# Performance work log

Hardware: AMD Instinct MI355X
Metric: run time of the kernel (lower is better)

The kernel has to match this reference:

```python
import jax, jax.numpy as jnp
import numpy as np

D_POINTS = 256
D_MODEL = 512
B, N = 8, 2048


def setup_inputs() -> dict:
    key = jax.random.key(0)
    ks = jax.random.split(key, 6)
    s_in = 1.0 / np.sqrt(D_POINTS)
    s_mid = 1.0 / np.sqrt(D_MODEL)
    return {
        "features": jax.random.normal(ks[0], (B, N, D_POINTS), dtype=jnp.float32),
        "Wq": jax.random.uniform(ks[1], (D_POINTS, D_MODEL), jnp.float32, -s_in, s_in),
        "Wk": jax.random.uniform(ks[2], (D_POINTS, D_MODEL), jnp.float32, -s_in, s_in),
        "Wv": jax.random.uniform(ks[3], (D_POINTS, D_MODEL), jnp.float32, -s_in, s_in),
        "W2": jax.random.uniform(ks[4], (D_MODEL, D_POINTS), jnp.float32, -s_mid, s_mid),
        "b2": jax.random.uniform(ks[5], (D_POINTS,), jnp.float32, -s_mid, s_mid),
    }


def reference(features, Wq, Wk, Wv, W2, b2):
    # features: [B, N, d_points]
    q = jnp.einsum("bnd,dm->bnm", features, Wq)  # [B, N, d_model]
    k = jnp.einsum("bnd,dm->bnm", features, Wk)
    v = jnp.einsum("bnd,dm->bnm", features, Wv)
    scale = 1.0 / np.sqrt(k.shape[-1]).astype(np.float32)
    attn = jax.nn.softmax(jnp.einsum("bnm,bkm->bnk", q, k) * scale, axis=-1)  # [B, N, N]
    res = jnp.einsum("bnk,bkm->bnm", attn, v)  # [B, N, d_model]
    res = jnp.einsum("bnm,md->bnd", res, W2) + b2  # fc2 -> [B, N, d_points]
    res = jax.nn.leaky_relu(res, negative_slope=0.2)
    return res + features
```

## Files before the change

kernel.cpp:

```cpp
#include <hip/hip_runtime.h>
#include <cstdint>

#define NBATCH 8
#define NSEQ   2048
#define NROWS  16384

typedef __attribute__((ext_vector_type(4))) float  f32x4;
typedef __attribute__((ext_vector_type(8))) short  short8;
typedef __attribute__((ext_vector_type(8))) __bf16 bf16x8;
typedef __attribute__((ext_vector_type(8))) _Float16 h8;

#define XB_OFF   0ul
#define WALL_OFF 8388608ul
#define Q_OFF    9175040ul
#define K_OFF    25952256ul
#define VT_OFF   42729472ul
#define W2T_OFF  59506688ul
#define S_OFF    59768832ul

#define SCALE_Q 0.063758746f

__device__ __forceinline__ unsigned short f2bf(float f) {
  unsigned u = __builtin_bit_cast(unsigned, f);
  return (unsigned short)((u + 0x7fffu + ((u >> 16) & 1u)) >> 16);
}

__device__ __forceinline__ f32x4 mfma16(short8 a, short8 b, f32x4 c) {
  return __builtin_amdgcn_mfma_f32_16x16x32_bf16(
      __builtin_bit_cast(bf16x8, a), __builtin_bit_cast(bf16x8, b), c, 0, 0, 0);
}

__device__ __forceinline__ void glds16(const void* g, void* l) {
  __builtin_amdgcn_global_load_lds(
      (const __attribute__((address_space(1))) void*)g,
      (__attribute__((address_space(3))) void*)l, 16, 0, 0);
}

#define BAR_SYNC()                     \
  {                                    \
    __builtin_amdgcn_sched_barrier(0); \
    __builtin_amdgcn_s_barrier();      \
    __builtin_amdgcn_sched_barrier(0); \
  }
#define BAR_LGKM()                                           \
  {                                                          \
    asm volatile("s_waitcnt lgkmcnt(0)" ::: "memory");       \
    __builtin_amdgcn_sched_barrier(0);                       \
    __builtin_amdgcn_s_barrier();                            \
    __builtin_amdgcn_sched_barrier(0);                       \
  }
#define WAITV(N)                                                  \
  {                                                               \
    asm volatile("s_waitcnt vmcnt(" #N ")" ::: "memory");         \
    __builtin_amdgcn_sched_barrier(0);                            \
  }

__global__ __launch_bounds__(256, 4) void prep_kernel(
    const float* __restrict__ feat, const float* __restrict__ Wq,
    const float* __restrict__ Wk, const float* __restrict__ Wv,
    const float* __restrict__ W2, char* __restrict__ ws) {
  int tid = blockIdx.x * 256 + threadIdx.x;
  if (tid < 524288) {
    int r = tid >> 5, co = (tid & 31) * 8;
    const float* src = feat + (size_t)r * 256 + co;
    short8 v;
#pragma unroll
    for (int i = 0; i < 8; ++i) v[i] = (short)f2bf(src[i]);
    unsigned short* Xb = (unsigned short*)(ws + XB_OFF);
    *(short8*)(Xb + (size_t)r * 256 + (co ^ ((r & 7) << 3))) = v;
  } else if (tid < 917504) {
    int t2 = tid - 524288;
    int m = t2 >> 8, d = t2 & 255;
    int wsel = m >> 9, mm = m & 511;
    const float* W = (wsel == 0) ? Wq : ((wsel == 1) ? Wk : Wv);
    float v = W[(size_t)d * 512 + mm];
    if (wsel == 0) v *= SCALE_Q;
    unsigned short* Wall = (unsigned short*)(ws + WALL_OFF);
    Wall[(size_t)m * 256 + (d ^ ((m & 7) << 3))] = f2bf(v);
  } else {
    int t3 = tid - 917504;
    int d = t3 >> 9, c = t3 & 511;
    unsigned short* W2t = (unsigned short*)(ws + W2T_OFF);
    W2t[(size_t)d * 512 + c] = f2bf(W2[(size_t)c * 256 + d]);
  }
}

__global__ __launch_bounds__(256, 2) void proj_kernel(char* __restrict__ ws) {
  __shared__ char smem[65536];
  const int tid = threadIdx.x;
  const int l = tid & 63, w = tid >> 6;
  const int g = l >> 4, m16 = l & 15;
  const int orig = blockIdx.x;
  const int wgid = (orig & 7) * 192 + (orig >> 3);
  const int nt = wgid % 12, mtb = wgid / 12;
  const char* XbT = ws + XB_OFF + (size_t)mtb * 65536;
  const char* WallT = ws + WALL_OFF + (size_t)nt * 65536;

  auto stage = [&](int buf, int kt) {
#pragma unroll
    for (int j = 0; j < 4; ++j) {
      int idx = j * 256 + tid;
      int r = idx >> 3, p = idx & 7;
      glds16(XbT + r * 512 + kt * 128 + p * 16, smem + buf * 16384 + idx * 16);
      glds16(WallT + r * 512 + kt * 128 + p * 16,
             smem + 32768 + buf * 16384 + idx * 16);
    }
  };

  const int mr = (w >> 1) * 64, nr = (w & 1) * 64;
  const int fxor = (m16 & 7) << 4;
  const f32x4 fz = {0.f, 0.f, 0.f, 0.f};
  f32x4 acc[4][4];
#pragma unroll
  for (int i = 0; i < 4; ++i)
#pragma unroll
    for (int j = 0; j < 4; ++j) acc[i][j] = fz;

  stage(0, 0);
  int cur = 0;
#pragma unroll 1
  for (int kt = 0; kt < 4; ++kt) {
    if (kt < 3) {
      stage(cur ^ 1, kt + 1);
      WAITV(8);
    } else {
      WAITV(0);
    }
    BAR_SYNC();
    const char* Ab = smem + cur * 16384;
    const char* Bb = smem + 32768 + cur * 16384;
#pragma unroll
    for (int ks = 0; ks < 2; ++ks) {
      int off = (16 * g + 64 * ks) ^ fxor;
      short8 af[4], bf[4];
#pragma unroll
      for (int i = 0; i < 4; ++i)
        af[i] = *(const short8*)(Ab + (mr + i * 16 + m16) * 128 + off);
#pragma unroll
      for (int i = 0; i < 4; ++i)
        bf[i] = *(const short8*)(Bb + (nr + i * 16 + m16) * 128 + off);
#pragma unroll
      for (int mi = 0; mi < 4; ++mi)
#pragma unroll
        for (int ni = 0; ni < 4; ++ni)
          acc[mi][ni] = mfma16(af[mi], bf[ni], acc[mi][ni]);
    }
    BAR_LGKM();
    cur ^= 1;
  }

  const int colg = nt * 128 + nr;
  const int tcat = colg >> 9;
  const int cin_base = colg & 511;
  char* wbuf = smem + w * 2048;
  if (tcat < 2) {
    char* dst = ws + (tcat == 0 ? Q_OFF : K_OFF) +
                ((size_t)(mtb * 8 + (cin_base >> 6))) * 16384;
#pragma unroll
    for (int mi = 0; mi < 4; ++mi) {
#pragma unroll
      for (int ni = 0; ni < 4; ++ni)
#pragma unroll
        for (int j = 0; j < 4; ++j) {
          int r = g * 4 + j, c = ni * 16 + m16;
          *(unsigned short*)(wbuf + r * 128 + ((2 * c) ^ ((r & 7) << 4))) =
              f2bf(acc[mi][ni][j]);
        }
      asm volatile("s_waitcnt lgkmcnt(0)" ::: "memory");
      __builtin_amdgcn_sched_barrier(0);
#pragma unroll
      for (int s = 0; s < 2; ++s) {
        int cid = l + 64 * s;
        int r2 = cid >> 3, gi = cid & 7;
        short8 v = *(const short8*)(wbuf + r2 * 128 + gi * 16);
        int rt = mr + mi * 16 + r2;
        *(short8*)(dst + (size_t)rt * 128 + gi * 16) = v;
      }
    }
  } else {
    short8 grans[8];
#pragma unroll
    for (int mi = 0; mi < 4; ++mi) {
#pragma unroll
      for (int ni = 0; ni < 4; ++ni)
#pragma unroll
        for (int j = 0; j < 4; ++j) {
          int r = g * 4 + j, c = ni * 16 + m16;
          *(unsigned short*)(wbuf + r * 128 + ((2 * c) ^ ((r & 7) << 4))) =
              f2bf(acc[mi][ni][j]);
        }
      asm volatile("s_waitcnt lgkmcnt(0)" ::: "memory");
      __builtin_amdgcn_sched_barrier(0);
      unsigned short vals[16];
#pragma unroll
      for (int r2 = 0; r2 < 16; ++r2)
        vals[r2] = *(const unsigned short*)(wbuf + r2 * 128 +
                                            ((2 * l) ^ ((r2 & 7) << 4)));
      short8 v0, v1;
#pragma unroll
      for (int i2 = 0; i2 < 8; ++i2) {
        v0[i2] = (short)vals[i2];
        v1[i2] = (short)vals[8 + i2];
      }
      grans[2 * mi] = v0;
      grans[2 * mi + 1] = v1;
    }
    int cin = cin_base + l;
    int grow0 = mtb * 128 + mr;
    int bb = grow0 >> 11;
    int ktv = (grow0 & 2047) >> 6;
    char* vrow = ws + VT_OFF + (size_t)bb * 2097152 + (size_t)ktv * 65536 +
                 (size_t)cin * 128;
    const int fc = (cin & 7) << 4;
#pragma unroll
    for (int t = 0; t < 8; ++t)
      *(short8*)(vrow + ((t * 16) ^ fc)) = grans[t];
  }
}

__global__ __launch_bounds__(256, 2) void qk_kernel(
    const char* __restrict__ ws, char* __restrict__ Sb, int nb, int b0) {
  __shared__ char smem[65536];
  const int tid = threadIdx.x;
  const int bid = blockIdx.x;
  const int z = bid % nb, tile = bid / nb;
  const int mt = tile >> 4, ntq = tile & 15;
  const int b = b0 + z;
  const int l = tid & 63, w = tid >> 6;
  const int g = l >> 4, m16 = l & 15;
  const int fxor = (m16 & 7) << 4;
  const char* Qt = ws + Q_OFF + (size_t)(b * 16 + mt) * 131072;
  const char* Kt = ws + K_OFF + (size_t)(b * 16 + ntq) * 131072;

  auto stage = [&](int buf, int kt) {
#pragma unroll
    for (int j = 0; j < 4; ++j) {
      int idx = j * 256 + tid;
      glds16(Qt + (size_t)kt * 16384 + idx * 16, smem + buf * 16384 + idx * 16);
      glds16(Kt + (size_t)kt * 16384 + idx * 16,
             smem + 32768 + buf * 16384 + idx * 16);
    }
  };

  const int mr = (w >> 1) * 64, nr = (w & 1) * 64;
  const f32x4 fz = {0.f, 0.f, 0.f, 0.f};
  f32x4 acc[4][4];
#pragma unroll
  for (int i = 0; i < 4; ++i)
#pragma unroll
    for (int j = 0; j < 4; ++j) acc[i][j] = fz;

  stage(0, 0);
  int cur = 0;
#pragma unroll 1
  for (int kt = 0; kt < 8; ++kt) {
    if (kt < 7) {
      stage(cur ^ 1, kt + 1);
      WAITV(8);
    } else {
      WAITV(0);
    }
    BAR_SYNC();
    const char* Ab = smem + cur * 16384;
    const char* Bb = smem + 32768 + cur * 16384;
#pragma unroll
    for (int ks = 0; ks < 2; ++ks) {
      int off = (16 * g + 64 * ks) ^ fxor;
      short8 af[4], bf[4];
#pragma unroll
      for (int i = 0; i < 4; ++i)
        af[i] = *(const short8*)(Ab + (mr + i * 16 + m16) * 128 + off);
#pragma unroll
      for (int i = 0; i < 4; ++i)
        bf[i] = *(const short8*)(Bb + (nr + i * 16 + m16) * 128 + off);
#pragma unroll
      for (int mi = 0; mi < 4; ++mi)
#pragma unroll
        for (int ni = 0; ni < 4; ++ni)
          acc[mi][ni] = mfma16(af[mi], bf[ni], acc[mi][ni]);
    }
    BAR_LGKM();
    cur ^= 1;
  }

#pragma unroll
  for (int mi = 0; mi < 4; ++mi)
#pragma unroll
    for (int ni = 0; ni < 4; ++ni)
#pragma unroll
      for (int j = 0; j < 4; ++j) {
        int r = mr + mi * 16 + g * 4 + j, c = nr + ni * 16 + m16;
        *(unsigned short*)(smem + r * 272 + 2 * c) =
            __builtin_bit_cast(unsigned short, (_Float16)acc[mi][ni][j]);
      }
  BAR_LGKM();
  char* Sbt = Sb + (size_t)z * 8388608;
#pragma unroll
  for (int it = 0; it < 8; ++it) {
    int idx = it * 256 + tid;
    int r = idx >> 4, gi = idx & 15;
    int rg = mt * 2 + (r >> 6), ck = ntq * 2 + (gi >> 3);
    *(short8*)(Sbt + ((size_t)(rg * 32 + ck) * 64 + (r & 63)) * 128 +
               (gi & 7) * 16) = *(const short8*)(smem + r * 272 + gi * 16);
  }
}

__global__ __launch_bounds__(256, 8) void stats_kernel(char* __restrict__ Sb) {
  const int w = threadIdx.x >> 6, l = threadIdx.x & 63;
  const size_t row = (size_t)blockIdx.x * 4 + w;
  const int z = (int)(row >> 11), rloc = (int)(row & 2047);
  const int rg = rloc >> 6, r64 = rloc & 63;
  const int f = (rloc & 7) << 4;
  char* base = Sb + (size_t)z * 8388608 + (size_t)rg * 262144 +
               (size_t)r64 * 128;
  float sv[32];
#pragma unroll
  for (int i = 0; i < 4; ++i) {
    int idx = i * 64 + l;
    int ck = idx >> 3, gi = idx & 7;
    h8 hv = *(const h8*)(base + (size_t)ck * 8192 + gi * 16);
#pragma unroll
    for (int j = 0; j < 8; ++j) sv[i * 8 + j] = (float)hv[j];
  }
  float m = sv[0];
#pragma unroll
  for (int i = 1; i < 32; ++i) m = fmaxf(m, sv[i]);
  m = fmaxf(m, __shfl_xor(m, 1));
  m = fmaxf(m, __shfl_xor(m, 2));
  m = fmaxf(m, __shfl_xor(m, 4));
  m = fmaxf(m, __shfl_xor(m, 8));
  m = fmaxf(m, __shfl_xor(m, 16));
  m = fmaxf(m, __shfl_xor(m, 32));
  float sum = 0.f;
#pragma unroll
  for (int i = 0; i < 32; ++i) {
    float p = exp2f(sv[i] - m);
    sv[i] = p;
    sum += p;
  }
  sum += __shfl_xor(sum, 1);
  sum += __shfl_xor(sum, 2);
  sum += __shfl_xor(sum, 4);
  sum += __shfl_xor(sum, 8);
  sum += __shfl_xor(sum, 16);
  sum += __shfl_xor(sum, 32);
  const float rs = 1.0f / sum;
#pragma unroll
  for (int i = 0; i < 4; ++i) {
    int idx = i * 64 + l;
    int ck = idx >> 3, gi = idx & 7;
    short8 pk;
#pragma unroll
    for (int j = 0; j < 8; ++j) pk[j] = (short)f2bf(sv[i * 8 + j] * rs);
    *(short8*)(base + (size_t)ck * 8192 + ((gi * 16) ^ f)) = pk;
  }
}

__global__ __launch_bounds__(512, 2) void pv_kernel(
    const char* __restrict__ ws, const char* __restrict__ Sb,
    const float* __restrict__ feat, const float* __restrict__ b2,
    float* __restrict__ out, int nb, int b0) {
  __shared__ char smem[147456];
  const int tid = threadIdx.x;
  const int bid = blockIdx.x;
  const int z = bid % nb, mt64 = bid / nb;
  const int b = b0 + z;
  const int l = tid & 63, w = tid >> 6;
  const int g = l >> 4, m16 = l & 15;
  const int fxor = (m16 & 7) << 4;
  const char* Pr = Sb + (size_t)z * 8388608 + (size_t)mt64 * 262144;
  const char* Vt = ws + VT_OFF + (size_t)b * 2097152;

  auto stage = [&](int buf, int kt) {
    glds16(Pr + (size_t)kt * 8192 + tid * 16, smem + buf * 8192 + tid * 16);
#pragma unroll
    for (int j = 0; j < 8; ++j) {
      int idx = j * 512 + tid;
      glds16(Vt + (size_t)kt * 65536 + idx * 16,
             smem + 16384 + buf * 65536 + idx * 16);
    }
  };

  const f32x4 fz = {0.f, 0.f, 0.f, 0.f};
  f32x4 acc[4][4];
#pragma unroll
  for (int i = 0; i < 4; ++i)
#pragma unroll
    for (int j = 0; j < 4; ++j) acc[i][j] = fz;

  stage(0, 0);
  int cur = 0;
#pragma unroll 1
  for (int kt = 0; kt < 32; ++kt) {
    if (kt < 31) {
      stage(cur ^ 1, kt + 1);
      WAITV(9);
    } else {
      WAITV(0);
    }
    BAR_SYNC();
    const char* Ab = smem + cur * 8192;
    const char* Vb = smem + 16384 + cur * 65536 + w * 8192;
#pragma unroll
    for (int ks = 0; ks < 2; ++ks) {
      int off = (16 * g + 64 * ks) ^ fxor;
      short8 af[4], vf[4];
#pragma unroll
      for (int i = 0; i < 4; ++i)
        af[i] = *(const short8*)(Ab + (i * 16 + m16) * 128 + off);
#pragma unroll
      for (int i = 0; i < 4; ++i)
        vf[i] = *(const short8*)(Vb + (i * 16 + m16) * 128 + off);
#pragma unroll
      for (int mi = 0; mi < 4; ++mi)
#pragma unroll
        for (int ni = 0; ni < 4; ++ni)
          acc[mi][ni] = mfma16(af[mi], vf[ni], acc[mi][ni]);
    }
    BAR_LGKM();
    cur ^= 1;
  }

  char* Ob = smem + 16384;
#pragma unroll
  for (int mi = 0; mi < 4; ++mi)
#pragma unroll
    for (int ni = 0; ni < 4; ++ni)
#pragma unroll
      for (int j = 0; j < 4; ++j) {
        int r = mi * 16 + g * 4 + j;
        int c = w * 64 + ni * 16 + m16;
        *(unsigned short*)(Ob + r * 1024 + ((2 * c) ^ ((r & 7) << 4))) =
            f2bf(acc[mi][ni][j]);
      }
  BAR_LGKM();

  const char* W2g = ws + W2T_OFF;
  f32x4 y[4][2];
#pragma unroll
  for (int i = 0; i < 4; ++i) {
    y[i][0] = fz;
    y[i][1] = fz;
  }
#pragma unroll 1
  for (int ks = 0; ks < 16; ++ks) {
    int off = (ks * 64 + 16 * g);
    short8 aa[4], wb[2];
#pragma unroll
    for (int mi2 = 0; mi2 < 4; ++mi2) {
      int r = mi2 * 16 + m16;
      aa[mi2] = *(const short8*)(Ob + r * 1024 + (off ^ fxor));
    }
#pragma unroll
    for (int ni2 = 0; ni2 < 2; ++ni2) {
      int d = w * 32 + ni2 * 16 + m16;
      wb[ni2] = *(const short8*)(W2g + (size_t)d * 1024 + ks * 64 + g * 16);
    }
#pragma unroll
    for (int mi2 = 0; mi2 < 4; ++mi2)
#pragma unroll
      for (int ni2 = 0; ni2 < 2; ++ni2)
        y[mi2][ni2] = mfma16(aa[mi2], wb[ni2], y[mi2][ni2]);
  }
#pragma unroll
  for (int mi2 = 0; mi2 < 4; ++mi2)
#pragma unroll
    for (int ni2 = 0; ni2 < 2; ++ni2) {
      int d = w * 32 + ni2 * 16 + m16;
      float bias = b2[d];
#pragma unroll
      for (int j = 0; j < 4; ++j) {
        size_t gr = (size_t)b * 2048 + mt64 * 64 + mi2 * 16 + g * 4 + j;
        float v = y[mi2][ni2][j] + bias;
        v = v > 0.f ? v : 0.2f * v;
        out[gr * 256 + d] = v + feat[gr * 256 + d];
      }
    }
}

extern "C" void kernel_launch(void* const* d_in, const int* in_sizes, int n_in,
                              void* d_out, int out_size, void* d_ws, size_t ws_size,
                              hipStream_t stream) {
  const float* feat = (const float*)d_in[0];
  const float* Wq = (const float*)d_in[1];
  const float* Wk = (const float*)d_in[2];
  const float* Wv = (const float*)d_in[3];
  const float* W2 = (const float*)d_in[4];
  const float* b2 = (const float*)d_in[5];
  float* out = (float*)d_out;
  char* ws = (char*)d_ws;
  (void)in_sizes; (void)n_in; (void)out_size;

  prep_kernel<<<4096, 256, 0, stream>>>(feat, Wq, Wk, Wv, W2, ws);
  proj_kernel<<<1536, 256, 0, stream>>>(ws);

  const size_t per_batch = 8388608ul;
  int nb = 8;
  while (nb > 1 && S_OFF + (size_t)nb * per_batch > ws_size) nb >>= 1;
  char* Sb = ws + S_OFF;
  for (int b0 = 0; b0 < 8; b0 += nb) {
    qk_kernel<<<256 * nb, 256, 0, stream>>>(ws, Sb, nb, b0);
    stats_kernel<<<512 * nb, 256, 0, stream>>>(Sb);
    pv_kernel<<<32 * nb, 512, 0, stream>>>(ws, Sb, feat, b2, out, nb, b0);
  }
}
```

Measured before the change: 160.4 us.

## Load K and V operands directly from global into registers, shrink LDS for occupancy

The projection kernel now writes K and V^T without the XOR swizzle, so the QK and PV kernels can load their B operands (K tiles and V^T tiles) straight from global memory into registers instead of staging them through shared memory. This cuts LDS usage (64KB to ~34KB in qk, 144KB to 64KB in pv), and the launch bounds are raised to allow 4 blocks per CU. The wait counts are adjusted for the extra outstanding vector loads. The cost is that the direct global loads sit right before each barrier with little prefetch distance, so latency may be exposed, and redundant global/L2 traffic rises since multiple waves reload the same tiles.

```diff
diff --git a/kernel.cpp b/kernel.cpp
--- a/kernel.cpp
+++ b/kernel.cpp
@@ -172,7 +172,8 @@
       for (int s = 0; s < 2; ++s) {
         int cid = l + 64 * s;
         int r2 = cid >> 3, gi = cid & 7;
-        short8 v = *(const short8*)(wbuf + r2 * 128 + gi * 16);
+        int slot = (tcat == 0) ? gi : (gi ^ (r2 & 7));
+        short8 v = *(const short8*)(wbuf + r2 * 128 + slot * 16);
         int rt = mr + mi * 16 + r2;
         *(short8*)(dst + (size_t)rt * 128 + gi * 16) = v;
       }
@@ -211,16 +212,15 @@
     int ktv = (grow0 & 2047) >> 6;
     char* vrow = ws + VT_OFF + (size_t)bb * 2097152 + (size_t)ktv * 65536 +
                  (size_t)cin * 128;
-    const int fc = (cin & 7) << 4;
 #pragma unroll
     for (int t = 0; t < 8; ++t)
-      *(short8*)(vrow + ((t * 16) ^ fc)) = grans[t];
-  }
-}
-
-__global__ __launch_bounds__(256, 2) void qk_kernel(
+      *(short8*)(vrow + t * 16) = grans[t];
+  }
+}
+
+__global__ __launch_bounds__(256, 4) void qk_kernel(
     const char* __restrict__ ws, char* __restrict__ Sb, int nb, int b0) {
-  __shared__ char smem[65536];
+  __shared__ char smem[34816];
   const int tid = threadIdx.x;
   const int bid = blockIdx.x;
   const int z = bid % nb, tile = bid / nb;
@@ -237,8 +237,6 @@
     for (int j = 0; j < 4; ++j) {
       int idx = j * 256 + tid;
       glds16(Qt + (size_t)kt * 16384 + idx * 16, smem + buf * 16384 + idx * 16);
-      glds16(Kt + (size_t)kt * 16384 + idx * 16,
-             smem + 32768 + buf * 16384 + idx * 16);
     }
   };
 
@@ -254,30 +252,34 @@
   int cur = 0;
 #pragma unroll 1
   for (int kt = 0; kt < 8; ++kt) {
+    short8 bf[2][4];
+#pragma unroll
+    for (int ks = 0; ks < 2; ++ks)
+#pragma unroll
+      for (int i = 0; i < 4; ++i)
+        bf[ks][i] = *(const short8*)(Kt + (size_t)kt * 16384 +
+                                     (nr + i * 16 + m16) * 128 + ks * 64 +
+                                     g * 16);
     if (kt < 7) {
       stage(cur ^ 1, kt + 1);
+      WAITV(12);
+    } else {
       WAITV(8);
-    } else {
-      WAITV(0);
     }
     BAR_SYNC();
     const char* Ab = smem + cur * 16384;
-    const char* Bb = smem + 32768 + cur * 16384;
 #pragma unroll
     for (int ks = 0; ks < 2; ++ks) {
       int off = (16 * g + 64 * ks) ^ fxor;
-      short8 af[4], bf[4];
+      short8 af[4];
 #pragma unroll
       for (int i = 0; i < 4; ++i)
         af[i] = *(const short8*)(Ab + (mr + i * 16 + m16) * 128 + off);
 #pragma unroll
-      for (int i = 0; i < 4; ++i)
-        bf[i] = *(const short8*)(Bb + (nr + i * 16 + m16) * 128 + off);
-#pragma unroll
       for (int mi = 0; mi < 4; ++mi)
 #pragma unroll
         for (int ni = 0; ni < 4; ++ni)
-          acc[mi][ni] = mfma16(af[mi], bf[ni], acc[mi][ni]);
+          acc[mi][ni] = mfma16(af[mi], bf[ks][ni], acc[mi][ni]);
     }
     BAR_LGKM();
     cur ^= 1;
@@ -356,11 +358,11 @@
   }
 }
 
-__global__ __launch_bounds__(512, 2) void pv_kernel(
+__global__ __launch_bounds__(512, 4) void pv_kernel(
     const char* __restrict__ ws, const char* __restrict__ Sb,
     const float* __restrict__ feat, const float* __restrict__ b2,
     float* __restrict__ out, int nb, int b0) {
-  __shared__ char smem[147456];
+  __shared__ char smem[65536];
   const int tid = threadIdx.x;
   const int bid = blockIdx.x;
   const int z = bid % nb, mt64 = bid / nb;
@@ -373,12 +375,6 @@
 
   auto stage = [&](int buf, int kt) {
     glds16(Pr + (size_t)kt * 8192 + tid * 16, smem + buf * 8192 + tid * 16);
-#pragma unroll
-    for (int j = 0; j < 8; ++j) {
-      int idx = j * 512 + tid;
-      glds16(Vt + (size_t)kt * 65536 + idx * 16,
-             smem + 16384 + buf * 65536 + idx * 16);
-    }
   };
 
   const f32x4 fz = {0.f, 0.f, 0.f, 0.f};
@@ -392,36 +388,40 @@
   int cur = 0;
 #pragma unroll 1
   for (int kt = 0; kt < 32; ++kt) {
+    const char* Vk = Vt + (size_t)kt * 65536;
+    short8 vf[2][4];
+#pragma unroll
+    for (int ks = 0; ks < 2; ++ks)
+#pragma unroll
+      for (int i = 0; i < 4; ++i)
+        vf[ks][i] = *(const short8*)(Vk + (w * 64 + i * 16 + m16) * 128 +
+                                     ks * 64 + g * 16);
     if (kt < 31) {
       stage(cur ^ 1, kt + 1);
       WAITV(9);
     } else {
-      WAITV(0);
+      WAITV(8);
     }
     BAR_SYNC();
     const char* Ab = smem + cur * 8192;
-    const char* Vb = smem + 16384 + cur * 65536 + w * 8192;
 #pragma unroll
     for (int ks = 0; ks < 2; ++ks) {
       int off = (16 * g + 64 * ks) ^ fxor;
-      short8 af[4], vf[4];
+      short8 af[4];
 #pragma unroll
       for (int i = 0; i < 4; ++i)
         af[i] = *(const short8*)(Ab + (i * 16 + m16) * 128 + off);
 #pragma unroll
-      for (int i = 0; i < 4; ++i)
-        vf[i] = *(const short8*)(Vb + (i * 16 + m16) * 128 + off);
-#pragma unroll
       for (int mi = 0; mi < 4; ++mi)
 #pragma unroll
         for (int ni = 0; ni < 4; ++ni)
-          acc[mi][ni] = mfma16(af[mi], vf[ni], acc[mi][ni]);
+          acc[mi][ni] = mfma16(af[mi], vf[ks][ni], acc[mi][ni]);
     }
     BAR_LGKM();
     cur ^= 1;
   }
 
-  char* Ob = smem + 16384;
+  char* Ob = smem;
 #pragma unroll
   for (int mi = 0; mi < 4; ++mi)
 #pragma unroll
```

Measured after the change: 218.9 us. +36.5%, slower.
